# Kernel tuning notes

Measured on AMD Instinct MI355X. Metric: run time of the kernel, lower is better.

## Reference

```python
import jax, jax.numpy as jnp
import numpy as np

EPS = 1e-8


def setup_inputs() -> dict:
    key = jax.random.key(0)
    k1, k2, k3 = jax.random.split(key, 3)
    T, B, d, n = 1024, 8, 64, 64
    v = jax.random.normal(k1, (T, B, d), dtype=jnp.float32)
    k = jax.random.normal(k2, (T, B, n), dtype=jnp.float32)
    alpha = jax.random.uniform(k3, (T, B, n), dtype=jnp.float32)
    return {"v": v, "k": k, "alpha": alpha}


def reference(v, k, alpha):
    # v: (T,B,d), k: (T,B,n), alpha: (T,B,n) in [0,1] -> S: (T,B,d,n)
    outer = jnp.einsum('tbd,tbn->tbdn', v, k)          # (T,B,d,n)
    log_alpha = jnp.log(jnp.maximum(alpha, EPS))       # clamp_min(1e-8)
    cumprod = jnp.exp(jnp.cumsum(log_alpha, axis=0))   # (T,B,n)
    decay = cumprod / (cumprod[-1:] + EPS)             # normalize by last step
    weighted = outer * decay[:, :, None, :]            # (T,B,d,n)
    S = jnp.cumsum(weighted, axis=0)
    return S
```

## Files before the change

kernel.cpp:

```cpp
#include <hip/hip_runtime.h>

#define T_DIM 1024
#define B_DIM 8
#define D_DIM 64
#define N_DIM 64

#define DC_CHUNKS 64
#define DC_LEN 16

#define SC_CHUNKS 16
#define SC_LEN 64

#define WS_W 0
#define WS_LSUM 524288
#define WS_PSUM 557056

__global__ __launch_bounds__(64) void decay_chunksum_kernel(
    const float* __restrict__ alpha, float* __restrict__ ws) {
  const int b = blockIdx.x >> 6;
  const int c = blockIdx.x & 63;
  const int n = threadIdx.x;

  float s = 0.f;
#pragma unroll
  for (int i = 0; i < DC_LEN; ++i) {
    const int t = c * DC_LEN + i;
    const float a = alpha[((size_t)t * B_DIM + b) * N_DIM + n];
    s += logf(fmaxf(a, 1e-8f));
  }
  ws[WS_LSUM + ((size_t)b * DC_CHUNKS + c) * N_DIM + n] = s;
}

__global__ __launch_bounds__(64) void decay_w_kernel(
    const float* __restrict__ alpha, const float* __restrict__ kk,
    float* __restrict__ ws) {
  const int b = blockIdx.x >> 6;
  const int c = blockIdx.x & 63;
  const int n = threadIdx.x;

  const float* __restrict__ lsum = ws + WS_LSUM + (size_t)b * DC_CHUNKS * N_DIM + n;
  float pre = 0.f, tot = 0.f;
#pragma unroll 8
  for (int j = 0; j < DC_CHUNKS; ++j) {
    const float sj = lsum[(size_t)j * N_DIM];
    pre += (j < c) ? sj : 0.f;
    tot += sj;
  }

  const float invden = 1.0f / (expf(tot) + 1e-8f);

  float cum = pre;
#pragma unroll
  for (int i = 0; i < DC_LEN; ++i) {
    const int t = c * DC_LEN + i;
    const size_t idx = ((size_t)t * B_DIM + b) * N_DIM + n;
    cum += logf(fmaxf(alpha[idx], 1e-8f));
    ws[WS_W + idx] = kk[idx] * expf(cum) * invden;
  }
}

__global__ __launch_bounds__(256) void chunk_psum_kernel(
    const float* __restrict__ v, const float* __restrict__ ws_in,
    float* __restrict__ ws_out) {
  const int bid = blockIdx.x;
  const int dt = bid & 3;
  const int b  = (bid >> 2) & 7;
  const int c  = bid >> 5;
  const int tid = threadIdx.x;
  const int d  = dt * 16 + (tid >> 4);
  const int n0 = (tid & 15) * 4;

  const float* __restrict__ vp = v + (size_t)b * D_DIM + d;
  const float* __restrict__ wp = ws_in + WS_W + (size_t)b * N_DIM + n0;

  float4 a0 = {0,0,0,0}, a1 = {0,0,0,0}, a2 = {0,0,0,0}, a3 = {0,0,0,0};
#pragma unroll 4
  for (int i = 0; i < SC_LEN; i += 4) {
    const int t = c * SC_LEN + i;
#pragma unroll
    for (int u = 0; u < 4; ++u) {
      const float vv = vp[(size_t)(t + u) * (B_DIM * D_DIM)];
      const float4 w4 = *(const float4*)(wp + (size_t)(t + u) * (B_DIM * N_DIM));
      float4& acc = (u == 0) ? a0 : (u == 1) ? a1 : (u == 2) ? a2 : a3;
      acc.x = fmaf(vv, w4.x, acc.x);
      acc.y = fmaf(vv, w4.y, acc.y);
      acc.z = fmaf(vv, w4.z, acc.z);
      acc.w = fmaf(vv, w4.w, acc.w);
    }
  }
  float4 s;
  s.x = (a0.x + a1.x) + (a2.x + a3.x);
  s.y = (a0.y + a1.y) + (a2.y + a3.y);
  s.z = (a0.z + a1.z) + (a2.z + a3.z);
  s.w = (a0.w + a1.w) + (a2.w + a3.w);
  *(float4*)(ws_out + WS_PSUM +
             (((size_t)c * B_DIM + b) * D_DIM + d) * N_DIM + n0) = s;
}

__global__ __launch_bounds__(256) void scan_store_kernel(
    const float* __restrict__ v, const float* __restrict__ ws,
    float* __restrict__ out) {
  const int bid = blockIdx.x;
  const int dt = bid & 3;
  const int b  = (bid >> 2) & 7;
  const int c  = bid >> 5;
  const int tid = threadIdx.x;
  const int d  = dt * 16 + (tid >> 4);
  const int n0 = (tid & 15) * 4;

  const float* __restrict__ vp = v + (size_t)b * D_DIM + d;
  const float* __restrict__ wp = ws + WS_W + (size_t)b * N_DIM + n0;
  const float* __restrict__ pp = ws + WS_PSUM + ((size_t)b * D_DIM + d) * N_DIM + n0;

  float4 acc = {0,0,0,0};
  for (int j = 0; j < c; ++j) {
    const float4 p = *(const float4*)(pp + (size_t)j * (B_DIM * D_DIM * N_DIM));
    acc.x += p.x; acc.y += p.y; acc.z += p.z; acc.w += p.w;
  }

#pragma unroll 8
  for (int i = 0; i < SC_LEN; ++i) {
    const int t = c * SC_LEN + i;
    const float vv = vp[(size_t)t * (B_DIM * D_DIM)];
    const float4 w4 = *(const float4*)(wp + (size_t)t * (B_DIM * N_DIM));
    acc.x = fmaf(vv, w4.x, acc.x);
    acc.y = fmaf(vv, w4.y, acc.y);
    acc.z = fmaf(vv, w4.z, acc.z);
    acc.w = fmaf(vv, w4.w, acc.w);
    *(float4*)(out + (((size_t)t * B_DIM + b) * D_DIM + d) * N_DIM + n0) = acc;
  }
}

extern "C" void kernel_launch(void* const* d_in, const int* in_sizes, int n_in,
                              void* d_out, int out_size, void* d_ws, size_t ws_size,
                              hipStream_t stream) {
  const float* v     = (const float*)d_in[0];
  const float* k     = (const float*)d_in[1];
  const float* alpha = (const float*)d_in[2];
  float* out = (float*)d_out;
  float* ws  = (float*)d_ws;

  decay_chunksum_kernel<<<B_DIM * DC_CHUNKS, 64, 0, stream>>>(alpha, ws);
  decay_w_kernel<<<B_DIM * DC_CHUNKS, 64, 0, stream>>>(alpha, k, ws);
  chunk_psum_kernel<<<SC_CHUNKS * B_DIM * 4, 256, 0, stream>>>(v, ws, ws);
  scan_store_kernel<<<SC_CHUNKS * B_DIM * 4, 256, 0, stream>>>(v, ws, out);
}
```

Measured before the change: 161.5 us.

## Fuse decay kernels into one block per batch, double scan chunks, nontemporal stores

The two decay kernels are merged into a single 1024-thread kernel per batch that keeps chunk log-sums in shared memory, removing one launch and a workspace round trip. When the workspace is large enough, the scan stage uses 32 time chunks instead of 16, doubling the grid to 1024 blocks for more parallelism at the cost of a longer prefix-sum loop. Output stores become nontemporal to avoid cache pollution on the large write stream. The fused decay kernel now runs only 8 blocks, which limits its parallelism.

```diff
diff --git a/kernel.cpp b/kernel.cpp
--- a/kernel.cpp
+++ b/kernel.cpp
@@ -5,63 +5,62 @@
 #define D_DIM 64
 #define N_DIM 64
 
-#define DC_CHUNKS 64
-#define DC_LEN 16
-
-#define SC_CHUNKS 16
-#define SC_LEN 64
+typedef float v4f __attribute__((ext_vector_type(4)));
 
 #define WS_W 0
-#define WS_LSUM 524288
-#define WS_PSUM 557056
+#define WS_PSUM 524288
 
-__global__ __launch_bounds__(64) void decay_chunksum_kernel(
-    const float* __restrict__ alpha, float* __restrict__ ws) {
-  const int b = blockIdx.x >> 6;
-  const int c = blockIdx.x & 63;
-  const int n = threadIdx.x;
-
-  float s = 0.f;
-#pragma unroll
-  for (int i = 0; i < DC_LEN; ++i) {
-    const int t = c * DC_LEN + i;
-    const float a = alpha[((size_t)t * B_DIM + b) * N_DIM + n];
-    s += logf(fmaxf(a, 1e-8f));
-  }
-  ws[WS_LSUM + ((size_t)b * DC_CHUNKS + c) * N_DIM + n] = s;
-}
-
-__global__ __launch_bounds__(64) void decay_w_kernel(
+template <int C>
+__global__ __launch_bounds__(1024) void decay_w_kernel(
     const float* __restrict__ alpha, const float* __restrict__ kk,
     float* __restrict__ ws) {
-  const int b = blockIdx.x >> 6;
-  const int c = blockIdx.x & 63;
-  const int n = threadIdx.x;
+  constexpr int LEN = T_DIM / C;
+  constexpr int CPT = C / 16;
+  const int b = blockIdx.x;
+  const int tid = threadIdx.x;
+  const int n = tid & 63;
+  const int ci = tid >> 6;
 
-  const float* __restrict__ lsum = ws + WS_LSUM + (size_t)b * DC_CHUNKS * N_DIM + n;
-  float pre = 0.f, tot = 0.f;
+  __shared__ float ls[C][N_DIM];
+
+#pragma unroll
+  for (int cc = 0; cc < CPT; ++cc) {
+    const int c = cc * 16 + ci;
+    float s = 0.f;
 #pragma unroll 8
-  for (int j = 0; j < DC_CHUNKS; ++j) {
-    const float sj = lsum[(size_t)j * N_DIM];
-    pre += (j < c) ? sj : 0.f;
-    tot += sj;
+    for (int i = 0; i < LEN; ++i) {
+      const int t = c * LEN + i;
+      s += logf(fmaxf(alpha[((size_t)t * B_DIM + b) * N_DIM + n], 1e-8f));
+    }
+    ls[c][n] = s;
   }
+  __syncthreads();
 
-  const float invden = 1.0f / (expf(tot) + 1e-8f);
-
-  float cum = pre;
 #pragma unroll
-  for (int i = 0; i < DC_LEN; ++i) {
-    const int t = c * DC_LEN + i;
-    const size_t idx = ((size_t)t * B_DIM + b) * N_DIM + n;
-    cum += logf(fmaxf(alpha[idx], 1e-8f));
-    ws[WS_W + idx] = kk[idx] * expf(cum) * invden;
+  for (int cc = 0; cc < CPT; ++cc) {
+    const int c = cc * 16 + ci;
+    float pre = 0.f, tot = 0.f;
+#pragma unroll
+    for (int j = 0; j < C; ++j) {
+      const float sv = ls[j][n];
+      tot += sv;
+      if (j < c) pre += sv;
+    }
+    const float invden = 1.0f / (expf(tot) + 1e-8f);
+    float cum = pre;
+#pragma unroll 4
+    for (int i = 0; i < LEN; ++i) {
+      const size_t idx = ((size_t)(c * LEN + i) * B_DIM + b) * N_DIM + n;
+      cum += logf(fmaxf(alpha[idx], 1e-8f));
+      ws[WS_W + idx] = kk[idx] * expf(cum) * invden;
+    }
   }
 }
 
+template <int C>
 __global__ __launch_bounds__(256) void chunk_psum_kernel(
-    const float* __restrict__ v, const float* __restrict__ ws_in,
-    float* __restrict__ ws_out) {
+    const float* __restrict__ v, float* __restrict__ ws) {
+  constexpr int LEN = T_DIM / C;
   const int bid = blockIdx.x;
   const int dt = bid & 3;
   const int b  = (bid >> 2) & 7;
@@ -71,35 +70,27 @@
   const int n0 = (tid & 15) * 4;
 
   const float* __restrict__ vp = v + (size_t)b * D_DIM + d;
-  const float* __restrict__ wp = ws_in + WS_W + (size_t)b * N_DIM + n0;
+  const float* __restrict__ wp = ws + WS_W + (size_t)b * N_DIM + n0;
 
-  float4 a0 = {0,0,0,0}, a1 = {0,0,0,0}, a2 = {0,0,0,0}, a3 = {0,0,0,0};
-#pragma unroll 4
-  for (int i = 0; i < SC_LEN; i += 4) {
-    const int t = c * SC_LEN + i;
-#pragma unroll
-    for (int u = 0; u < 4; ++u) {
-      const float vv = vp[(size_t)(t + u) * (B_DIM * D_DIM)];
-      const float4 w4 = *(const float4*)(wp + (size_t)(t + u) * (B_DIM * N_DIM));
-      float4& acc = (u == 0) ? a0 : (u == 1) ? a1 : (u == 2) ? a2 : a3;
-      acc.x = fmaf(vv, w4.x, acc.x);
-      acc.y = fmaf(vv, w4.y, acc.y);
-      acc.z = fmaf(vv, w4.z, acc.z);
-      acc.w = fmaf(vv, w4.w, acc.w);
-    }
+  v4f acc = {0.f, 0.f, 0.f, 0.f};
+#pragma unroll 8
+  for (int i = 0; i < LEN; ++i) {
+    const int t = c * LEN + i;
+    const float vv = vp[(size_t)t * (B_DIM * D_DIM)];
+    const v4f w4 = *(const v4f*)(wp + (size_t)t * (B_DIM * N_DIM));
+    acc.x = fmaf(vv, w4.x, acc.x);
+    acc.y = fmaf(vv, w4.y, acc.y);
+    acc.z = fmaf(vv, w4.z, acc.z);
+    acc.w = fmaf(vv, w4.w, acc.w);
   }
-  float4 s;
-  s.x = (a0.x + a1.x) + (a2.x + a3.x);
-  s.y = (a0.y + a1.y) + (a2.y + a3.y);
-  s.z = (a0.z + a1.z) + (a2.z + a3.z);
-  s.w = (a0.w + a1.w) + (a2.w + a3.w);
-  *(float4*)(ws_out + WS_PSUM +
-             (((size_t)c * B_DIM + b) * D_DIM + d) * N_DIM + n0) = s;
+  *(v4f*)(ws + WS_PSUM + (((size_t)c * B_DIM + b) * D_DIM + d) * N_DIM + n0) = acc;
 }
 
+template <int C>
 __global__ __launch_bounds__(256) void scan_store_kernel(
     const float* __restrict__ v, const float* __restrict__ ws,
     float* __restrict__ out) {
+  constexpr int LEN = T_DIM / C;
   const int bid = blockIdx.x;
   const int dt = bid & 3;
   const int b  = (bid >> 2) & 7;
@@ -112,22 +103,24 @@
   const float* __restrict__ wp = ws + WS_W + (size_t)b * N_DIM + n0;
   const float* __restrict__ pp = ws + WS_PSUM + ((size_t)b * D_DIM + d) * N_DIM + n0;
 
-  float4 acc = {0,0,0,0};
+  v4f acc = {0.f, 0.f, 0.f, 0.f};
+#pragma unroll 4
   for (int j = 0; j < c; ++j) {
-    const float4 p = *(const float4*)(pp + (size_t)j * (B_DIM * D_DIM * N_DIM));
+    const v4f p = *(const v4f*)(pp + (size_t)j * (B_DIM * D_DIM * N_DIM));
     acc.x += p.x; acc.y += p.y; acc.z += p.z; acc.w += p.w;
   }
 
 #pragma unroll 8
-  for (int i = 0; i < SC_LEN; ++i) {
-    const int t = c * SC_LEN + i;
+  for (int i = 0; i < LEN; ++i) {
+    const int t = c * LEN + i;
     const float vv = vp[(size_t)t * (B_DIM * D_DIM)];
-    const float4 w4 = *(const float4*)(wp + (size_t)t * (B_DIM * N_DIM));
+    const v4f w4 = *(const v4f*)(wp + (size_t)t * (B_DIM * N_DIM));
     acc.x = fmaf(vv, w4.x, acc.x);
     acc.y = fmaf(vv, w4.y, acc.y);
     acc.z = fmaf(vv, w4.z, acc.z);
     acc.w = fmaf(vv, w4.w, acc.w);
-    *(float4*)(out + (((size_t)t * B_DIM + b) * D_DIM + d) * N_DIM + n0) = acc;
+    __builtin_nontemporal_store(
+        acc, (v4f*)(out + (((size_t)t * B_DIM + b) * D_DIM + d) * N_DIM + n0));
   }
 }
 
@@ -140,8 +133,14 @@
   float* out = (float*)d_out;
   float* ws  = (float*)d_ws;
 
-  decay_chunksum_kernel<<<B_DIM * DC_CHUNKS, 64, 0, stream>>>(alpha, ws);
-  decay_w_kernel<<<B_DIM * DC_CHUNKS, 64, 0, stream>>>(alpha, k, ws);
-  chunk_psum_kernel<<<SC_CHUNKS * B_DIM * 4, 256, 0, stream>>>(v, ws, ws);
-  scan_store_kernel<<<SC_CHUNKS * B_DIM * 4, 256, 0, stream>>>(v, ws, out);
+  const size_t needed32 = (size_t)(WS_PSUM + 32 * B_DIM * D_DIM * N_DIM) * sizeof(float);
+  if (ws_size >= needed32) {
+    decay_w_kernel<32><<<B_DIM, 1024, 0, stream>>>(alpha, k, ws);
+    chunk_psum_kernel<32><<<32 * 32, 256, 0, stream>>>(v, ws);
+    scan_store_kernel<32><<<32 * 32, 256, 0, stream>>>(v, ws, out);
+  } else {
+    decay_w_kernel<16><<<B_DIM, 1024, 0, stream>>>(alpha, k, ws);
+    chunk_psum_kernel<16><<<16 * 32, 256, 0, stream>>>(v, ws);
+    scan_store_kernel<16><<<16 * 32, 256, 0, stream>>>(v, ws, out);
+  }
 }
```

New measurement: 183.1 us. +13.4%, slower.
